# Performance work log

Hardware: AMD Instinct MI355X
Metric: run time of the kernel (lower is better)

## Reference

```python
import jax, jax.numpy as jnp
import numpy as np

BS = 4
D = 256
N3 = BS * 80 * 80   # 25600 level-3 nodes
N4 = BS * 40 * 40   # 6400  level-4 nodes
N5 = BS * 20 * 20   # 1600  level-5 nodes
N = N3 + N4 + N5    # 33600 total graph nodes
EC = 260000         # contextual-graph edges (~8-neighborhood lattice)
EH = 120000         # hierarchical-graph edges (cross-scale)


def setup_inputs() -> dict:
    key = jax.random.key(0)
    ks = jax.random.split(key, 16)
    f = lambda k, s: jax.random.normal(k, s, dtype=jnp.float32) * 0.05
    return {
        # backbone features (yolov8-l channel widths)
        'c3': f(ks[0], (BS, 256, 80, 80)),
        'c4': f(ks[1], (BS, 512, 40, 40)),
        'c5': f(ks[2], (BS, 512, 20, 20)),
        # lateral 1x1 convs (stored as [out, in] since kernel is 1x1)
        'w3_1x1': f(ks[3], (256, 256)), 'b3_1x1': jnp.zeros((256,), jnp.float32),
        'w4_1x1': f(ks[4], (256, 512)), 'b4_1x1': jnp.zeros((256,), jnp.float32),
        'w5_1x1': f(ks[5], (256, 512)), 'b5_1x1': jnp.zeros((256,), jnp.float32),
        # output 3x3 convs
        'w3_3x3': f(ks[6], (256, 256, 3, 3)), 'b3_3x3': jnp.zeros((256,), jnp.float32),
        'w4_3x3': f(ks[7], (256, 256, 3, 3)), 'b4_3x3': jnp.zeros((256,), jnp.float32),
        'w5_3x3': f(ks[8], (256, 256, 3, 3)), 'b5_3x3': jnp.zeros((256,), jnp.float32),
        # 6 contextual + 3 hierarchical GNN layers (stacked)
        'Wc': f(ks[9], (6, 256, 256)), 'bc': jnp.zeros((6, 256), jnp.float32),
        'Wh': f(ks[10], (3, 256, 256)), 'bh': jnp.zeros((3, 256), jnp.float32),
        # edge lists (src -> dst message direction)
        'src_c': jax.random.randint(ks[11], (EC,), 0, N, dtype=jnp.int32),
        'dst_c': jax.random.randint(ks[12], (EC,), 0, N, dtype=jnp.int32),
        'src_h': jax.random.randint(ks[13], (EH,), 0, N, dtype=jnp.int32),
        'dst_h': jax.random.randint(ks[14], (EH,), 0, N, dtype=jnp.int32),
    }


def _conv1x1(x, w, b):
    return jnp.einsum('bchw,oc->bohw', x, w) + b[None, :, None, None]


def _conv3x3(x, w, b):
    y = jax.lax.conv_general_dilated(x, w, (1, 1), 'SAME')
    return y + b[None, :, None, None]


def _up2(x):
    return jnp.repeat(jnp.repeat(x, 2, axis=2), 2, axis=3)


def _degree(dst):
    d = jax.ops.segment_sum(jnp.ones(dst.shape, jnp.float32), dst, num_segments=N)
    return jnp.maximum(d, 1.0)[:, None]


def _gnn_layer(h, W, b, src, dst, deg):
    # gather-aggregate-scatter: mean over incoming messages + self, then linear+relu
    agg = jax.ops.segment_sum(h[src], dst, num_segments=N) / deg  # [N, D]
    return jax.nn.relu((h + agg) @ W + b)


def reference(c3, c4, c5,
              w3_1x1, b3_1x1, w4_1x1, b4_1x1, w5_1x1, b5_1x1,
              w3_3x3, b3_3x3, w4_3x3, b4_3x3, w5_3x3, b5_3x3,
              Wc, bc, Wh, bh,
              src_c, dst_c, src_h, dst_h):
    p3 = _conv1x1(c3, w3_1x1, b3_1x1)  # [BS,256,80,80]
    p4 = _conv1x1(c4, w4_1x1, b4_1x1)  # [BS,256,40,40]
    p5 = _conv1x1(c5, w5_1x1, b5_1x1)  # [BS,256,20,20]

    # CNN -> graph node features (NHWC flatten, cat levels)
    h = jnp.concatenate([
        p3.transpose(0, 2, 3, 1).reshape(-1, D),
        p4.transpose(0, 2, 3, 1).reshape(-1, D),
        p5.transpose(0, 2, 3, 1).reshape(-1, D),
    ], axis=0)  # [N, 256]

    deg_c = _degree(dst_c)
    deg_h = _degree(dst_h)
    for i in range(3):                       # context1..3
        h = _gnn_layer(h, Wc[i], bc[i], src_c, dst_c, deg_c)
    for i in range(3):                       # hierarch1..3
        h = _gnn_layer(h, Wh[i], bh[i], src_h, dst_h, deg_h)
    for i in range(3, 6):                    # context4..6
        h = _gnn_layer(h, Wc[i], bc[i], src_c, dst_c, deg_c)

    # graph -> CNN
    p3g = h[:N3].reshape(BS, 80, 80, D).transpose(0, 3, 1, 2)
    p4g = h[N3:N3 + N4].reshape(BS, 40, 40, D).transpose(0, 3, 1, 2)
    p5g = h[N3 + N4:].reshape(BS, 20, 20, D).transpose(0, 3, 1, 2)

    p5 = p5 + p5g
    p4 = p4 + _up2(p5) + p4g
    p3 = p3 + _up2(p4) + p3g

    out3 = _conv3x3(p3, w3_3x3, b3_3x3)
    out4 = _conv3x3(p4, w4_3x3, b4_3x3)
    out5 = _conv3x3(p5, w5_3x3, b5_3x3)
    return out3, out4, out5
```

## Files before the change

### kernel.cpp

```cpp
#include <hip/hip_runtime.h>
#include <stdint.h>

#define N3i 25600
#define N4i 6400
#define N5i 1600
#define NNi 33600
#define ECi 260000
#define EHi 120000

typedef unsigned short u16;
typedef __bf16 bf16x8 __attribute__((ext_vector_type(8)));
typedef float f32x4 __attribute__((ext_vector_type(4)));
typedef unsigned short u16x8 __attribute__((ext_vector_type(8)));

__device__ __forceinline__ float b2f(u16 u) {
    union { float f; uint32_t i; } v; v.i = ((uint32_t)u) << 16; return v.f;
}
__device__ __forceinline__ u16 f2b(float f) {
    union { float f; uint32_t i; } v; v.f = f;
    uint32_t x = v.i;
    uint32_t r = (x + 0x7FFFu + ((x >> 16) & 1u)) >> 16;
    return (u16)r;
}

__device__ __forceinline__ void gll16(const u16* g, u16* l) {
    __builtin_amdgcn_global_load_lds((const __attribute__((address_space(1))) void*)g,
                                     (__attribute__((address_space(3))) void*)l, 16, 0, 0);
}

__device__ __forceinline__ bool xcd_pair_decode(int pid, int& p, int& x) {
    int g = pid & 7;
    int s = pid >> 3;
    x = s & 1;
    p = g * 33 + (s >> 1);
    return p < 263;
}

__global__ void detect_kernel(const void* __restrict__ c3raw, int* __restrict__ flag,
                              uint32_t* __restrict__ zp) {
    const uint32_t* p = (const uint32_t*)c3raw;
    int t = threadIdx.x;
    zp[t] = 0;
    int vote = 0;
    for (int i = t; i < 256; i += 64) {
        uint32_t w = p[i];
        uint32_t lo = w & 0xFFFFu;
        uint32_t e = (lo >> 7) & 0xFFu;
        if (lo == 0u || (e >= 100u && e <= 127u)) vote++;
    }
#pragma unroll
    for (int d = 32; d >= 1; d >>= 1) vote += __shfl_down(vote, d, 64);
    if (t == 0) flag[0] = (vote >= 192) ? 1 : 0;
}

__global__ void zero_i32(int* p, int n) {
    int i = blockIdx.x * 256 + threadIdx.x;
    if (i < n) p[i] = 0;
}

__global__ void hist2_kernel(const int* __restrict__ dst_c, const int* __restrict__ dst_h,
                             int* __restrict__ cnt_c, int* __restrict__ cnt_h) {
    int i = blockIdx.x * 256 + threadIdx.x;
    if (i < ECi) {
        int d = dst_c[i];
        if ((unsigned)d < (unsigned)NNi) atomicAdd(&cnt_c[d], 1);
    } else {
        int j = i - ECi;
        if (j < EHi) {
            int d = dst_h[j];
            if ((unsigned)d < (unsigned)NNi) atomicAdd(&cnt_h[d], 1);
        }
    }
}

__global__ __launch_bounds__(1024) void scan2_kernel(
    const int* __restrict__ cnt_c, int* __restrict__ rs_c, int* __restrict__ cur_c,
    float* __restrict__ inv_c,
    const int* __restrict__ cnt_h, int* __restrict__ rs_h, int* __restrict__ cur_h,
    float* __restrict__ inv_h, int n) {
    const int* cnt = blockIdx.x ? cnt_h : cnt_c;
    int* rs = blockIdx.x ? rs_h : rs_c;
    int* cur = blockIdx.x ? cur_h : cur_c;
    float* inv = blockIdx.x ? inv_h : inv_c;
    __shared__ int ws[16];
    __shared__ int base;
    int t = threadIdx.x, wid = t >> 6, lane = t & 63;
    if (t == 0) { base = 0; rs[0] = 0; }
    __syncthreads();
    for (int i0 = 0; i0 < n; i0 += 1024) {
        int i = i0 + t;
        int v = (i < n) ? cnt[i] : 0;
        int x = v;
#pragma unroll
        for (int d = 1; d < 64; d <<= 1) {
            int y = __shfl_up(x, d, 64);
            if (lane >= d) x += y;
        }
        if (lane == 63) ws[wid] = x;
        __syncthreads();
        if (wid == 0) {
            int s = (lane < 16) ? ws[lane] : 0;
#pragma unroll
            for (int d = 1; d < 16; d <<= 1) {
                int y = __shfl_up(s, d, 64);
                if (lane >= d) s += y;
            }
            if (lane < 16) ws[lane] = s;
        }
        __syncthreads();
        int b = base;
        int incl = x + (wid ? ws[wid - 1] : 0);
        if (i < n) {
            rs[i + 1] = b + incl;
            cur[i] = b + incl - v;
            int dv = v < 1 ? 1 : v;
            inv[i] = 1.0f / (float)dv;
        }
        int tot = ws[15];
        __syncthreads();
        if (t == 1023) base = b + tot;
        __syncthreads();
    }
}

__global__ void fill2_kernel(const int* __restrict__ src_c, const int* __restrict__ dst_c,
                             int* __restrict__ cur_c, int* __restrict__ csr_c,
                             const int* __restrict__ src_h, const int* __restrict__ dst_h,
                             int* __restrict__ cur_h, int* __restrict__ csr_h) {
    int i = blockIdx.x * 256 + threadIdx.x;
    if (i < ECi) {
        int d = dst_c[i];
        if ((unsigned)d < (unsigned)NNi) {
            int p = atomicAdd(&cur_c[d], 1);
            if ((unsigned)p < (unsigned)ECi) csr_c[p] = src_c[i];
        }
    } else {
        int j = i - ECi;
        if (j < EHi) {
            int d = dst_h[j];
            if ((unsigned)d < (unsigned)NNi) {
                int p = atomicAdd(&cur_h[d], 1);
                if ((unsigned)p < (unsigned)EHi) csr_h[p] = src_h[j];
            }
        }
    }
}

struct CvtJobs { const void* src[11]; u16* dst[11]; int n[11]; };

__global__ void cvt_all_kernel(CvtJobs j, const int* __restrict__ flag) {
    int job = blockIdx.y;
    int i = blockIdx.x * 256 + threadIdx.x;
    if (i >= j.n[job]) return;
    const void* s = j.src[job];
    j.dst[job][i] = flag[0] ? ((const u16*)s)[i] : f2b(((const float*)s)[i]);
}

__device__ __forceinline__ void tin_body(const void* in, size_t ioff, u16* outp, int R, int C,
                                         int isb, int c0, int r0, u16 (*tile)[33]) {
    const u16* inb = (const u16*)in + ioff;
    const float* inf_ = (const float*)in + ioff;
    int tx = threadIdx.x, ty = threadIdx.y;
#pragma unroll
    for (int i = 0; i < 4; i++) {
        int r = r0 + ty + i * 8, c = c0 + tx;
        if (r < R && c < C) {
            size_t idx = (size_t)r * C + c;
            tile[ty + i * 8][tx] = isb ? inb[idx] : f2b(inf_[idx]);
        }
    }
    __syncthreads();
#pragma unroll
    for (int i = 0; i < 4; i++) {
        int c = c0 + ty + i * 8, r = r0 + tx;
        if (c < C && r < R) outp[(size_t)c * R + r] = tile[tx][ty + i * 8];
    }
}

__global__ void transpose_in3(const void* __restrict__ c3, const void* __restrict__ c4,
                              const void* __restrict__ c5, u16* __restrict__ Xt3,
                              u16* __restrict__ Xt4, u16* __restrict__ Xt5,
                              const int* __restrict__ flag) {
    __shared__ u16 tile[32][33];
    int bx = blockIdx.x;
    const void* in; u16* outb; int R, C, xb;
    if (bx < 200)      { in = c3; outb = Xt3; R = 256; C = 6400; xb = bx; }
    else if (bx < 250) { in = c4; outb = Xt4; R = 512; C = 1600; xb = bx - 200; }
    else               { in = c5; outb = Xt5; R = 512; C = 400;  xb = bx - 250; }
    int r0 = blockIdx.y * 32;
    if (r0 >= R) return;
    size_t boff = (size_t)blockIdx.z * R * C;
    tin_body(in, boff, outb + boff, R, C, flag[0], xb * 32, r0, tile);
}

__global__ void transpose_w(const void* __restrict__ Wc, const void* __restrict__ Wh,
                            u16* __restrict__ WtG, const int* __restrict__ flag) {
    __shared__ u16 tile[32][33];
    int z = blockIdx.z;
    const void* in = (z < 6) ? Wc : Wh;
    int zi = (z < 6) ? z : z - 6;
    tin_body(in, (size_t)zi * 65536, WtG + (size_t)z * 65536, 256, 256, flag[0],
             blockIdx.x * 32, blockIdx.y * 32, tile);
}

__global__ void transpose_out3(const u16* __restrict__ OutT, void* __restrict__ outv,
                               const int* __restrict__ flag) {
    __shared__ u16 tile[32][33];
    int by = blockIdx.y;
    const u16* inb; size_t out_off; int R, yb;
    if (by < 200)      { inb = OutT; out_off = 0; R = 6400; yb = by; }
    else if (by < 250) { inb = OutT + (size_t)N3i * 256; out_off = (size_t)4 * 256 * 6400; R = 1600; yb = by - 200; }
    else               { inb = OutT + (size_t)(N3i + N4i) * 256; out_off = (size_t)4 * 256 * 8000; R = 400; yb = by - 250; }
    int r0 = yb * 32;
    if (r0 >= R) return;
    const int C = 256;
    int isb = flag[0];
    int c0 = blockIdx.x * 32;
    size_t boff = (size_t)blockIdx.z * R * C;
    const u16* inp = inb + boff;
    int tx = threadIdx.x, ty = threadIdx.y;
#pragma unroll
    for (int i = 0; i < 4; i++) {
        int r = r0 + ty + i * 8, c = c0 + tx;
        if (r < R && c < C) tile[ty + i * 8][tx] = inp[(size_t)r * C + c];
    }
    __syncthreads();
#pragma unroll
    for (int i = 0; i < 4; i++) {
        int c = c0 + ty + i * 8, r = r0 + tx;
        if (c < C && r < R) {
            size_t o = out_off + boff + (size_t)c * R + r;
            u16 v = tile[tx][ty + i * 8];
            if (isb) ((u16*)outv)[o] = v;
            else ((float*)outv)[o] = b2f(v);
        }
    }
}

__global__ void convw3_kernel(const void* __restrict__ w0, const void* __restrict__ w1,
                              const void* __restrict__ w2, u16* __restrict__ WtC,
                              const int* __restrict__ flag) {
    int lvl = blockIdx.y;
    const void* w = (lvl == 0) ? w0 : (lvl == 1) ? w1 : w2;
    u16* wt = WtC + (size_t)lvl * 256 * 2304;
    int i = blockIdx.x * 256 + threadIdx.x;
    if (i >= 256 * 2304) return;
    int n = i / 2304;
    int k = i - n * 2304;
    int tap = k >> 8, ci = k & 255;
    int si = n * 2304 + ci * 9 + tap;
    wt[i] = flag[0] ? ((const u16*)w)[si] : f2b(((const float*)w)[si]);
}

__global__ __launch_bounds__(256) void gather_kernel(
    const u16* __restrict__ H, const int* __restrict__ csr, const int* __restrict__ rs,
    const float* __restrict__ invdeg, u16* __restrict__ T, int ecap) {
    int node = blockIdx.x * 8 + (threadIdx.x >> 5);
    if (node >= NNi) return;
    int L = threadIdx.x & 31;
    int c = L * 8;
    int e0 = rs[node], e1 = rs[node + 1];
    e0 = e0 < 0 ? 0 : e0;
    e1 = e1 > ecap ? ecap : e1;
    u16x8 self = *(const u16x8*)(H + (size_t)node * 256 + c);
    float a0 = 0.f, a1 = 0.f, a2 = 0.f, a3 = 0.f, a4 = 0.f, a5 = 0.f, a6 = 0.f, a7 = 0.f;
    float b0 = 0.f, b1 = 0.f, b2 = 0.f, b3 = 0.f, b4 = 0.f, b5 = 0.f, b6 = 0.f, b7 = 0.f;
    for (int base = e0; base < e1; base += 32) {
        int ee = base + L;
        int iv = 0;
        if (ee < e1) {
            iv = csr[ee];
            iv = ((unsigned)iv < (unsigned)NNi) ? iv : 0;
        }
        int cnt = e1 - base;
        cnt = cnt > 32 ? 32 : cnt;
        int k = 0;
        for (; k + 3 < cnt; k += 4) {
            int j0 = __shfl(iv, k, 32), j1 = __shfl(iv, k + 1, 32);
            int j2 = __shfl(iv, k + 2, 32), j3 = __shfl(iv, k + 3, 32);
            u16x8 h0 = *(const u16x8*)(H + (size_t)j0 * 256 + c);
            u16x8 h1 = *(const u16x8*)(H + (size_t)j1 * 256 + c);
            u16x8 h2 = *(const u16x8*)(H + (size_t)j2 * 256 + c);
            u16x8 h3 = *(const u16x8*)(H + (size_t)j3 * 256 + c);
            a0 += b2f(h0[0]); a1 += b2f(h0[1]); a2 += b2f(h0[2]); a3 += b2f(h0[3]);
            a4 += b2f(h0[4]); a5 += b2f(h0[5]); a6 += b2f(h0[6]); a7 += b2f(h0[7]);
            b0 += b2f(h1[0]); b1 += b2f(h1[1]); b2 += b2f(h1[2]); b3 += b2f(h1[3]);
            b4 += b2f(h1[4]); b5 += b2f(h1[5]); b6 += b2f(h1[6]); b7 += b2f(h1[7]);
            a0 += b2f(h2[0]); a1 += b2f(h2[1]); a2 += b2f(h2[2]); a3 += b2f(h2[3]);
            a4 += b2f(h2[4]); a5 += b2f(h2[5]); a6 += b2f(h2[6]); a7 += b2f(h2[7]);
            b0 += b2f(h3[0]); b1 += b2f(h3[1]); b2 += b2f(h3[2]); b3 += b2f(h3[3]);
            b4 += b2f(h3[4]); b5 += b2f(h3[5]); b6 += b2f(h3[6]); b7 += b2f(h3[7]);
        }
        if (k + 1 < cnt) {
            int j0 = __shfl(iv, k, 32), j1 = __shfl(iv, k + 1, 32);
            u16x8 h0 = *(const u16x8*)(H + (size_t)j0 * 256 + c);
            u16x8 h1 = *(const u16x8*)(H + (size_t)j1 * 256 + c);
            a0 += b2f(h0[0]); a1 += b2f(h0[1]); a2 += b2f(h0[2]); a3 += b2f(h0[3]);
            a4 += b2f(h0[4]); a5 += b2f(h0[5]); a6 += b2f(h0[6]); a7 += b2f(h0[7]);
            b0 += b2f(h1[0]); b1 += b2f(h1[1]); b2 += b2f(h1[2]); b3 += b2f(h1[3]);
            b4 += b2f(h1[4]); b5 += b2f(h1[5]); b6 += b2f(h1[6]); b7 += b2f(h1[7]);
            k += 2;
        }
        if (k < cnt) {
            int j0 = __shfl(iv, k, 32);
            u16x8 h0 = *(const u16x8*)(H + (size_t)j0 * 256 + c);
            a0 += b2f(h0[0]); a1 += b2f(h0[1]); a2 += b2f(h0[2]); a3 += b2f(h0[3]);
            a4 += b2f(h0[4]); a5 += b2f(h0[5]); a6 += b2f(h0[6]); a7 += b2f(h0[7]);
        }
    }
    a0 += b0; a1 += b1; a2 += b2; a3 += b3; a4 += b4; a5 += b5; a6 += b6; a7 += b7;
    float inv = invdeg[node];
    u16x8 o;
    o[0] = f2b(b2f(self[0]) + a0 * inv); o[1] = f2b(b2f(self[1]) + a1 * inv);
    o[2] = f2b(b2f(self[2]) + a2 * inv); o[3] = f2b(b2f(self[3]) + a3 * inv);
    o[4] = f2b(b2f(self[4]) + a4 * inv); o[5] = f2b(b2f(self[5]) + a5 * inv);
    o[6] = f2b(b2f(self[6]) + a6 * inv); o[7] = f2b(b2f(self[7]) + a7 * inv);
    *(u16x8*)(T + (size_t)node * 256 + c) = o;
}

template <bool CONV, bool RELU>
__device__ __forceinline__ void gemm_body(
    u16 (* __restrict__ lds)[4096],
    const u16* __restrict__ A, int lda,
    const u16* __restrict__ Bt, int ldb,
    const u16* __restrict__ bias,
    const u16* __restrict__ zp,
    u16* __restrict__ out, u16* __restrict__ out2,
    int M, int K, int H, int W, int m0, int n0) {
    int t = threadIdx.x;
    int w = t >> 6, lane = t & 63;
    int wm = w & 1, wn = w >> 1;
    f32x4 acc[4][4] = {};

    int g0 = w * 128 + lane;
    int g1 = g0 + 64;
    int row0 = g0 >> 2, c0 = g0 & 3;
    int row1 = g1 >> 2, c1 = g1 & 3;
    int ss0 = ((c0 ^ ((row0 >> 1) & 3)) << 3);
    int ss1 = ((c1 ^ ((row1 >> 1) & 3)) << 3);

    int ar0 = m0 + row0, ar1 = m0 + row1;
    bool aok0 = ar0 < M, aok1 = ar1 < M;
    int y0_ = 0, x0_ = 0, y1_ = 0, x1_ = 0;
    if (CONV) {
        int HW = H * W;
        if (aok0) { int b = ar0 / HW; int rem = ar0 - b * HW; y0_ = rem / W; x0_ = rem - y0_ * W; }
        if (aok1) { int b = ar1 / HW; int rem = ar1 - b * HW; y1_ = rem / W; x1_ = rem - y1_ * W; }
    }
    const u16* aP0 = A + (size_t)ar0 * lda + ss0;
    const u16* aP1 = A + (size_t)ar1 * lda + ss1;
    const u16* bP0 = Bt + (size_t)(n0 + row0) * ldb + ss0;
    const u16* bP1 = Bt + (size_t)(n0 + row1) * ldb + ss1;

    int lbase = w * 1024;

    auto stage = [&](int bf, int k0) {
        u16* LA = lds[bf * 2];
        u16* LB = lds[bf * 2 + 1];
        const u16* sa0;
        const u16* sa1;
        if (!CONV) {
            sa0 = aok0 ? aP0 + k0 : zp;
            sa1 = aok1 ? aP1 + k0 : zp;
        } else {
            int tap = k0 >> 8;
            int t3 = tap / 3;
            int dy = t3 - 1, dx = tap - t3 * 3 - 1;
            int off = (dy * W + dx) * lda + (k0 & 255);
            int yy0 = y0_ + dy, xx0 = x0_ + dx;
            int yy1 = y1_ + dy, xx1 = x1_ + dx;
            sa0 = (aok0 && (unsigned)yy0 < (unsigned)H && (unsigned)xx0 < (unsigned)W) ? aP0 + off : zp;
            sa1 = (aok1 && (unsigned)yy1 < (unsigned)H && (unsigned)xx1 < (unsigned)W) ? aP1 + off : zp;
        }
        gll16(sa0, LA + lbase);
        gll16(sa1, LA + lbase + 512);
        gll16(bP0 + k0, LB + lbase);
        gll16(bP1 + k0, LB + lbase + 512);
    };

    int nst = K >> 5;
    int fm = lane & 15;
    int co = (((lane >> 4) ^ ((fm >> 1) & 3)) << 3);

    stage(0, 0);
    __syncthreads();
    for (int s = 0; s < nst; s++) {
        int bf = s & 1;
        if (s + 1 < nst) stage(bf ^ 1, (s + 1) << 5);
        const u16* LA = lds[bf * 2];
        const u16* LB = lds[bf * 2 + 1];
        bf16x8 af[4], bfv[4];
#pragma unroll
        for (int i = 0; i < 4; i++) af[i] = *(const bf16x8*)&LA[(wm * 64 + i * 16 + fm) * 32 + co];
#pragma unroll
        for (int j = 0; j < 4; j++) bfv[j] = *(const bf16x8*)&LB[(wn * 64 + j * 16 + fm) * 32 + co];
#pragma unroll
        for (int i = 0; i < 4; i++)
#pragma unroll
            for (int j = 0; j < 4; j++)
                acc[i][j] = __builtin_amdgcn_mfma_f32_16x16x32_bf16(af[i], bfv[j], acc[i][j], 0, 0, 0);
        __syncthreads();
    }

    int q = lane >> 4, nl = lane & 15;
#pragma unroll
    for (int j = 0; j < 4; j++) {
        int n = n0 + wn * 64 + j * 16 + nl;
        float bv = b2f(bias[n]);
#pragma unroll
        for (int i = 0; i < 4; i++) {
            int mbase = m0 + wm * 64 + i * 16 + q * 4;
#pragma unroll
            for (int rg = 0; rg < 4; rg++) {
                int m = mbase + rg;
                if (m < M) {
                    float v = acc[i][j][rg] + bv;
                    if (RELU) v = fmaxf(v, 0.f);
                    u16 bs = f2b(v);
                    out[(size_t)m * 256 + n] = bs;
                    if (out2) out2[(size_t)m * 256 + n] = bs;
                }
            }
        }
    }
}

template <bool CONV, bool RELU>
__global__ __launch_bounds__(256) void gemm_kernel(
    const u16* __restrict__ A, int lda,
    const u16* __restrict__ Bt, int ldb,
    const u16* __restrict__ bias,
    const u16* __restrict__ zp,
    u16* __restrict__ out, u16* __restrict__ out2,
    int M, int K, int H, int W) {
    __shared__ __align__(16) u16 lds[4][4096];
    int p, x;
    if (!xcd_pair_decode(blockIdx.x, p, x)) return;
    gemm_body<CONV, RELU>(lds, A, lda, Bt, ldb, bias, zp, out, out2, M, K, H, W,
                          p * 128, x * 128);
}

__global__ __launch_bounds__(256) void lat_all_kernel(
    const u16* __restrict__ Xt3, const u16* __restrict__ Xt4, const u16* __restrict__ Xt5,
    const u16* __restrict__ W1, const u16* __restrict__ BB, const u16* __restrict__ zp,
    u16* __restrict__ P, u16* __restrict__ Ha) {
    __shared__ __align__(16) u16 lds[4][4096];
    int p, x;
    if (!xcd_pair_decode(blockIdx.x, p, x)) return;
    const u16* A; const u16* Bt; const u16* bias;
    int K, Ml, m0; size_t off;
    if (p < 200)      { A = Xt3; Bt = W1;          bias = BB;       K = 256; Ml = N3i; off = 0;                          m0 = p * 128; }
    else if (p < 250) { A = Xt4; Bt = W1 + 65536;  bias = BB + 256; K = 512; Ml = N4i; off = (size_t)N3i * 256;          m0 = (p - 200) * 128; }
    else              { A = Xt5; Bt = W1 + 196608; bias = BB + 512; K = 512; Ml = N5i; off = (size_t)(N3i + N4i) * 256;  m0 = (p - 250) * 128; }
    gemm_body<false, false>(lds, A, K, Bt, K, bias, zp, P + off, Ha + off, Ml, K, 0, 0,
                            m0, x * 128);
}

__global__ __launch_bounds__(256) void conv_gemm_all(
    const u16* __restrict__ Pc, const u16* __restrict__ WtC,
    const u16* __restrict__ BB, const u16* __restrict__ zp, u16* __restrict__ OutT) {
    __shared__ __align__(16) u16 lds[4][4096];
    int p, x;
    if (!xcd_pair_decode(blockIdx.x, p, x)) return;
    int lvl, yl, Hd, Ml; size_t base;
    if (p < 200)      { lvl = 0; yl = p;       Hd = 80; Ml = N3i; base = 0; }
    else if (p < 250) { lvl = 1; yl = p - 200; Hd = 40; Ml = N4i; base = (size_t)N3i * 256; }
    else              { lvl = 2; yl = p - 250; Hd = 20; Ml = N5i; base = (size_t)(N3i + N4i) * 256; }
    gemm_body<true, false>(lds, Pc + base, 256, WtC + (size_t)lvl * 256 * 2304, 2304,
                           BB + 3072 + lvl * 256, zp, OutT + base, nullptr,
                           Ml, 2304, Hd, Hd, yl * 128, x * 128);
}

__global__ void pyr_kernel(const u16* __restrict__ P, const u16* __restrict__ Hf,
                           u16* __restrict__ Pc) {
    int i = blockIdx.x * 256 + threadIdx.x;
    if (i >= NNi * 64) return;
    int node = i >> 6, c = (i & 63) * 4;
    size_t bi = (size_t)node * 256 + c;
    ushort4 pv = *(const ushort4*)(P + bi);
    ushort4 hv = *(const ushort4*)(Hf + bi);
    float v0 = b2f(pv.x) + b2f(hv.x);
    float v1 = b2f(pv.y) + b2f(hv.y);
    float v2 = b2f(pv.z) + b2f(hv.z);
    float v3 = b2f(pv.w) + b2f(hv.w);
    if (node < N3i) {
        int b = node / 6400, rem = node - b * 6400;
        int y = rem / 80, x = rem - y * 80;
        size_t s4 = ((size_t)N3i + b * 1600 + (y >> 1) * 40 + (x >> 1)) * 256 + c;
        size_t s5 = ((size_t)(N3i + N4i) + b * 400 + (y >> 2) * 20 + (x >> 2)) * 256 + c;
        ushort4 p4 = *(const ushort4*)(P + s4), h4 = *(const ushort4*)(Hf + s4);
        ushort4 p5 = *(const ushort4*)(P + s5), h5 = *(const ushort4*)(Hf + s5);
        v0 += b2f(p4.x) + b2f(h4.x) + b2f(p5.x) + b2f(h5.x);
        v1 += b2f(p4.y) + b2f(h4.y) + b2f(p5.y) + b2f(h5.y);
        v2 += b2f(p4.z) + b2f(h4.z) + b2f(p5.z) + b2f(h5.z);
        v3 += b2f(p4.w) + b2f(h4.w) + b2f(p5.w) + b2f(h5.w);
    } else if (node < N3i + N4i) {
        int n4 = node - N3i;
        int b = n4 / 1600, rem = n4 - b * 1600;
        int y = rem / 40, x = rem - y * 40;
        size_t s5 = ((size_t)(N3i + N4i) + b * 400 + (y >> 1) * 20 + (x >> 1)) * 256 + c;
        ushort4 p5 = *(const ushort4*)(P + s5), h5 = *(const ushort4*)(Hf + s5);
        v0 += b2f(p5.x) + b2f(h5.x);
        v1 += b2f(p5.y) + b2f(h5.y);
        v2 += b2f(p5.z) + b2f(h5.z);
        v3 += b2f(p5.w) + b2f(h5.w);
    }
    ushort4 o;
    o.x = f2b(v0); o.y = f2b(v1); o.z = f2b(v2); o.w = f2b(v3);
    *(ushort4*)(Pc + bi) = o;
}

extern "C" void kernel_launch(void* const* d_in, const int* in_sizes, int n_in,
                              void* d_out, int out_size, void* d_ws, size_t ws_size,
                              hipStream_t stream) {
    (void)in_sizes; (void)n_in; (void)out_size; (void)ws_size;
    const void* c3 = d_in[0];
    const void* c4 = d_in[1];
    const void* c5 = d_in[2];
    const void* w3_1 = d_in[3];
    const void* b3_1 = d_in[4];
    const void* w4_1 = d_in[5];
    const void* b4_1 = d_in[6];
    const void* w5_1 = d_in[7];
    const void* b5_1 = d_in[8];
    const void* w3_3 = d_in[9];
    const void* b3_3 = d_in[10];
    const void* w4_3 = d_in[11];
    const void* b4_3 = d_in[12];
    const void* w5_3 = d_in[13];
    const void* b5_3 = d_in[14];
    const void* Wc = d_in[15];
    const void* bc = d_in[16];
    const void* Wh = d_in[17];
    const void* bh = d_in[18];
    const int* src_c = (const int*)d_in[19];
    const int* dst_c = (const int*)d_in[20];
    const int* src_h = (const int*)d_in[21];
    const int* dst_h = (const int*)d_in[22];

    char* w = (char*)d_ws;
    auto alloc = [&](size_t bytes) -> void* {
        void* p = (void*)w;
        w += (bytes + 255) & ~(size_t)255;
        return p;
    };
    u16* XT  = (u16*)alloc(((size_t)N3i * 256 + (size_t)N4i * 512 + (size_t)N5i * 512) * 2);
    u16* Xt3 = XT;
    u16* Xt4 = XT + (size_t)N3i * 256;
    u16* Xt5 = Xt4 + (size_t)N4i * 512;
    u16* T   = XT;
    u16* Pc  = XT;
    u16* WtC = XT + (size_t)NNi * 256;
    u16* WtG = (u16*)alloc((size_t)9 * 65536 * 2);
    u16* W1  = (u16*)alloc((size_t)(65536 + 131072 + 131072) * 2);
    u16* BB  = (u16*)alloc((size_t)3840 * 2);
    u16* P   = (u16*)alloc((size_t)NNi * 256 * 2);
    u16* Ha  = (u16*)alloc((size_t)NNi * 256 * 2);
    u16* Hb  = (u16*)d_out;
    int* csr_c = (int*)alloc((size_t)ECi * 4);
    int* csr_h = (int*)alloc((size_t)EHi * 4);
    int* cnt2  = (int*)alloc((size_t)2 * NNi * 4);
    int* cnt_c = cnt2;
    int* cnt_h = cnt2 + NNi;
    int* rs_c  = (int*)alloc((size_t)(NNi + 1) * 4);
    int* rs_h  = (int*)alloc((size_t)(NNi + 1) * 4);
    int* cur_c = (int*)alloc((size_t)NNi * 4);
    int* cur_h = (int*)alloc((size_t)NNi * 4);
    float* inv_c = (float*)alloc((size_t)NNi * 4);
    float* inv_h = (float*)alloc((size_t)NNi * 4);
    int* flag  = (int*)alloc(256);
    u16* zp    = (u16*)alloc(256);

    detect_kernel<<<1, 64, 0, stream>>>(c3, flag, (uint32_t*)zp);

    zero_i32<<<(2 * NNi + 255) / 256, 256, 0, stream>>>(cnt2, 2 * NNi);
    hist2_kernel<<<(ECi + EHi + 255) / 256, 256, 0, stream>>>(dst_c, dst_h, cnt_c, cnt_h);
    scan2_kernel<<<2, 1024, 0, stream>>>(cnt_c, rs_c, cur_c, inv_c,
                                         cnt_h, rs_h, cur_h, inv_h, NNi);
    fill2_kernel<<<(ECi + EHi + 255) / 256, 256, 0, stream>>>(
        src_c, dst_c, cur_c, csr_c, src_h, dst_h, cur_h, csr_h);

    CvtJobs cj;
    cj.src[0] = w3_1; cj.dst[0] = W1;          cj.n[0] = 65536;
    cj.src[1] = w4_1; cj.dst[1] = W1 + 65536;  cj.n[1] = 131072;
    cj.src[2] = w5_1; cj.dst[2] = W1 + 196608; cj.n[2] = 131072;
    cj.src[3] = b3_1; cj.dst[3] = BB;          cj.n[3] = 256;
    cj.src[4] = b4_1; cj.dst[4] = BB + 256;    cj.n[4] = 256;
    cj.src[5] = b5_1; cj.dst[5] = BB + 512;    cj.n[5] = 256;
    cj.src[6] = bc;   cj.dst[6] = BB + 768;    cj.n[6] = 1536;
    cj.src[7] = bh;   cj.dst[7] = BB + 2304;   cj.n[7] = 768;
    cj.src[8] = b3_3; cj.dst[8] = BB + 3072;   cj.n[8] = 256;
    cj.src[9] = b4_3; cj.dst[9] = BB + 3328;   cj.n[9] = 256;
    cj.src[10] = b5_3; cj.dst[10] = BB + 3584; cj.n[10] = 256;
    cvt_all_kernel<<<dim3(512, 11), 256, 0, stream>>>(cj, flag);

    transpose_in3<<<dim3(263, 16, 4), dim3(32, 8), 0, stream>>>(c3, c4, c5, Xt3, Xt4, Xt5, flag);
    transpose_w<<<dim3(8, 8, 9), dim3(32, 8), 0, stream>>>(Wc, Wh, WtG, flag);

    lat_all_kernel<<<528, 256, 0, stream>>>(Xt3, Xt4, Xt5, W1, BB, zp, P, Ha);

    convw3_kernel<<<dim3(2304, 3), 256, 0, stream>>>(w3_3, w4_3, w5_3, WtC, flag);

    u16* Hcur = Ha;
    u16* Hnxt = Hb;
    for (int l = 0; l < 9; l++) {
        bool ctx = (l < 3) || (l >= 6);
        const int* csr = ctx ? csr_c : csr_h;
        const int* rs = ctx ? rs_c : rs_h;
        const float* inv = ctx ? inv_c : inv_h;
        int ecap = ctx ? ECi : EHi;
        int wi = (l < 3) ? l : (l < 6 ? 6 + (l - 3) : l - 3);
        const u16* bias = (l < 3) ? BB + 768 + l * 256
                        : (l < 6 ? BB + 2304 + (l - 3) * 256 : BB + 768 + (l - 3) * 256);
        gather_kernel<<<NNi / 8, 256, 0, stream>>>(Hcur, csr, rs, inv, T, ecap);
        gemm_kernel<false, true><<<528, 256, 0, stream>>>(
            T, 256, WtG + (size_t)wi * 65536, 256, bias, zp, Hnxt, nullptr, NNi, 256, 0, 0);
        u16* tmp = Hcur; Hcur = Hnxt; Hnxt = tmp;
    }
    u16* OutT = Hnxt;

    pyr_kernel<<<(NNi * 64 + 255) / 256, 256, 0, stream>>>(P, Hcur, Pc);

    conv_gemm_all<<<528, 256, 0, stream>>>(Pc, WtC, BB, zp, OutT);

    transpose_out3<<<dim3(8, 263, 4), dim3(32, 8), 0, stream>>>(OutT, d_out, flag);
}
```

Before: 654.6 us.

## Parallelize degree prefix scan across blocks and swizzle gather block order

New measurement: 622.8 us. 1.05x faster.

```diff
diff --git a/kernel.cpp b/kernel.cpp
--- a/kernel.cpp
+++ b/kernel.cpp
@@ -73,54 +73,85 @@
     }
 }
 
-__global__ __launch_bounds__(1024) void scan2_kernel(
-    const int* __restrict__ cnt_c, int* __restrict__ rs_c, int* __restrict__ cur_c,
-    float* __restrict__ inv_c,
-    const int* __restrict__ cnt_h, int* __restrict__ rs_h, int* __restrict__ cur_h,
-    float* __restrict__ inv_h, int n) {
-    const int* cnt = blockIdx.x ? cnt_h : cnt_c;
-    int* rs = blockIdx.x ? rs_h : rs_c;
-    int* cur = blockIdx.x ? cur_h : cur_c;
-    float* inv = blockIdx.x ? inv_h : inv_c;
-    __shared__ int ws[16];
-    __shared__ int base;
-    int t = threadIdx.x, wid = t >> 6, lane = t & 63;
-    if (t == 0) { base = 0; rs[0] = 0; }
+__global__ __launch_bounds__(256) void scan_part(
+    const int* __restrict__ cnt_c, const int* __restrict__ cnt_h,
+    int* __restrict__ ps_c, int* __restrict__ ps_h, int* __restrict__ bsum) {
+    int b = blockIdx.x;
+    bool hier = b >= 66;
+    const int* cnt = hier ? cnt_h : cnt_c;
+    int* ps = hier ? ps_h : ps_c;
+    int base = (hier ? b - 66 : b) * 512;
+    int t = threadIdx.x, lane = t & 63, wid = t >> 6;
+    int i0 = base + 2 * t;
+    int v0 = (i0 < NNi) ? cnt[i0] : 0;
+    int v1 = (i0 + 1 < NNi) ? cnt[i0 + 1] : 0;
+    int s = v0 + v1;
+    int x = s;
+#pragma unroll
+    for (int d = 1; d < 64; d <<= 1) {
+        int y = __shfl_up(x, d, 64);
+        if (lane >= d) x += y;
+    }
+    __shared__ int ws[4];
+    if (lane == 63) ws[wid] = x;
     __syncthreads();
-    for (int i0 = 0; i0 < n; i0 += 1024) {
-        int i = i0 + t;
-        int v = (i < n) ? cnt[i] : 0;
-        int x = v;
-#pragma unroll
-        for (int d = 1; d < 64; d <<= 1) {
-            int y = __shfl_up(x, d, 64);
-            if (lane >= d) x += y;
-        }
-        if (lane == 63) ws[wid] = x;
+    int w0 = ws[0], w1 = ws[1], w2 = ws[2], w3 = ws[3];
+    int woff = (wid == 1) ? w0 : (wid == 2) ? (w0 + w1) : (wid == 3) ? (w0 + w1 + w2) : 0;
+    int incl = x + woff;
+    int excl = incl - s;
+    if (i0 < NNi) ps[i0] = excl + v0;
+    if (i0 + 1 < NNi) ps[i0 + 1] = excl + v0 + v1;
+    if (t == 0) bsum[b] = w0 + w1 + w2 + w3;
+}
+
+__global__ __launch_bounds__(256) void scan_sums(int* __restrict__ bsum) {
+    __shared__ int s[132];
+    int t = threadIdx.x;
+    int orig = 0;
+    if (t < 132) { orig = bsum[t]; s[t] = orig; }
+    __syncthreads();
+    for (int d = 1; d < 66; d <<= 1) {
+        int v = 0;
+        if (t < 132) {
+            int seg = (t < 66) ? 0 : 1;
+            int loc = t - seg * 66;
+            if (loc >= d) v = s[t - d];
+        }
         __syncthreads();
-        if (wid == 0) {
-            int s = (lane < 16) ? ws[lane] : 0;
-#pragma unroll
-            for (int d = 1; d < 16; d <<= 1) {
-                int y = __shfl_up(s, d, 64);
-                if (lane >= d) s += y;
-            }
-            if (lane < 16) ws[lane] = s;
-        }
+        if (t < 132) s[t] += v;
         __syncthreads();
-        int b = base;
-        int incl = x + (wid ? ws[wid - 1] : 0);
-        if (i < n) {
-            rs[i + 1] = b + incl;
-            cur[i] = b + incl - v;
-            int dv = v < 1 ? 1 : v;
-            inv[i] = 1.0f / (float)dv;
-        }
-        int tot = ws[15];
-        __syncthreads();
-        if (t == 1023) base = b + tot;
-        __syncthreads();
-    }
+    }
+    if (t < 132) bsum[t] = s[t] - orig;
+}
+
+__global__ __launch_bounds__(256) void scan_final(
+    const int* __restrict__ ps_c, const int* __restrict__ ps_h, const int* __restrict__ bsum,
+    const int* __restrict__ cnt_c, const int* __restrict__ cnt_h,
+    int* __restrict__ rs_c, int* __restrict__ cur_c, float* __restrict__ inv_c,
+    int* __restrict__ rs_h, int* __restrict__ cur_h, float* __restrict__ inv_h) {
+    int b = blockIdx.x;
+    bool hier = b >= 66;
+    int lb = hier ? b - 66 : b;
+    const int* ps = hier ? ps_h : ps_c;
+    const int* cnt = hier ? cnt_h : cnt_c;
+    int* rs = hier ? rs_h : rs_c;
+    int* cur = hier ? cur_h : cur_c;
+    float* inv = hier ? inv_h : inv_c;
+    int off = bsum[b];
+    int t = threadIdx.x;
+#pragma unroll
+    for (int k = 0; k < 2; k++) {
+        int i = lb * 512 + t + k * 256;
+        if (i < NNi) {
+            int incl = ps[i] + off;
+            int v = cnt[i];
+            rs[i + 1] = incl;
+            cur[i] = incl - v;
+            inv[i] = 1.0f / (float)(v < 1 ? 1 : v);
+        }
+    }
+    if (b == 0 && t == 0) rs_c[0] = 0;
+    if (b == 66 && t == 0) rs_h[0] = 0;
 }
 
 __global__ void fill2_kernel(const int* __restrict__ src_c, const int* __restrict__ dst_c,
@@ -255,7 +286,9 @@
 __global__ __launch_bounds__(256) void gather_kernel(
     const u16* __restrict__ H, const int* __restrict__ csr, const int* __restrict__ rs,
     const float* __restrict__ invdeg, u16* __restrict__ T, int ecap) {
-    int node = blockIdx.x * 8 + (threadIdx.x >> 5);
+    int bid = blockIdx.x;
+    int nb = (bid & 7) * 525 + (bid >> 3);
+    int node = nb * 8 + (threadIdx.x >> 5);
     if (node >= NNi) return;
     int L = threadIdx.x & 31;
     int c = L * 8;
@@ -568,6 +601,9 @@
     int* cur_h = (int*)alloc((size_t)NNi * 4);
     float* inv_c = (float*)alloc((size_t)NNi * 4);
     float* inv_h = (float*)alloc((size_t)NNi * 4);
+    int* ps_c  = (int*)alloc((size_t)NNi * 4);
+    int* ps_h  = (int*)alloc((size_t)NNi * 4);
+    int* bsum  = (int*)alloc((size_t)132 * 4);
     int* flag  = (int*)alloc(256);
     u16* zp    = (u16*)alloc(256);
 
@@ -575,8 +611,10 @@
 
     zero_i32<<<(2 * NNi + 255) / 256, 256, 0, stream>>>(cnt2, 2 * NNi);
     hist2_kernel<<<(ECi + EHi + 255) / 256, 256, 0, stream>>>(dst_c, dst_h, cnt_c, cnt_h);
-    scan2_kernel<<<2, 1024, 0, stream>>>(cnt_c, rs_c, cur_c, inv_c,
-                                         cnt_h, rs_h, cur_h, inv_h, NNi);
+    scan_part<<<132, 256, 0, stream>>>(cnt_c, cnt_h, ps_c, ps_h, bsum);
+    scan_sums<<<1, 256, 0, stream>>>(bsum);
+    scan_final<<<132, 256, 0, stream>>>(ps_c, ps_h, bsum, cnt_c, cnt_h,
+                                        rs_c, cur_c, inv_c, rs_h, cur_h, inv_h);
     fill2_kernel<<<(ECi + EHi + 255) / 256, 256, 0, stream>>>(
         src_c, dst_c, cur_c, csr_c, src_h, dst_h, cur_h, csr_h);
 
```
